# Kernel optimization log

Measured on AMD Instinct MI355X. Metric: run time of the kernel, lower is better.

The kernel has to match this reference:

```python
import jax, jax.numpy as jnp
import numpy as np

# Dimensions pinned by the module: RelPosEmb1DAISummer(tokens=50, dim_head=124)
H = 8          # num_heads
D = 31         # channels // num_heads
T = 4          # time axis of the (p, t) spatial grid; D*T == 124 == dim_head
P = 50         # tokens
C = H * D      # 248 channels
SCALE = D ** -0.5  # note: module scales by d**-0.5 (=31), not (d*t)**-0.5 -- faithful


def rel_to_abs(x):
    """AI-Summer 1D relative->absolute reindexing. x: [b, h, l, 2l-1] -> [b, h, l, l]."""
    b, h, l, _ = x.shape
    x = jnp.pad(x, ((0, 0), (0, 0), (0, 0), (0, 1)))          # [b,h,l,2l]
    x = x.reshape(b, h, l * 2 * l)
    x = jnp.pad(x, ((0, 0), (0, 0), (0, l - 1)))
    x = x.reshape(b, h, l + 1, 2 * l - 1)
    return x[:, :, :l, l - 1:]


def setup_inputs() -> dict:
    key = jax.random.key(0)
    k1, k2, k3, k4 = jax.random.split(key, 4)
    B = 512
    x = jax.random.normal(k1, (B, C, P, T), jnp.float32)
    # 1x1 conv == per-position linear over channels: weight [3C, C], bias [3C]
    w_qkv = jax.random.normal(k2, (3 * C, C), jnp.float32) * (C ** -0.5)
    b_qkv = jax.random.normal(k3, (3 * C,), jnp.float32) * 0.01
    # shared-heads relative position embedding: [2*tokens-1, dim_head]
    rel_emb = jax.random.normal(k4, (2 * P - 1, D * T), jnp.float32) * ((D * T) ** -0.5)
    return {"x": x, "w_qkv": w_qkv, "b_qkv": b_qkv, "rel_emb": rel_emb}


def reference(x, w_qkv, b_qkv, rel_emb):
    B = x.shape[0]
    # 1x1 Conv2d: [B, C, P, T] -> [B, 3C, P, T]
    qkv = jnp.einsum('bcpt,oc->bopt', x, w_qkv) + b_qkv[None, :, None, None]
    # 'b (qkv h d) p t -> qkv b h d p t'
    qkv = qkv.reshape(B, 3, H, D, P, T)
    q, k, v = qkv[:, 0], qkv[:, 1], qkv[:, 2]                 # each [B,H,D,P,T]
    q = q.transpose(0, 1, 3, 2, 4).reshape(B, H, P, D * T)    # 'b h d p t -> b h p (d t)'
    k = k.transpose(0, 1, 2, 4, 3).reshape(B, H, D * T, P)    # 'b h d p t -> b h (d t) p'
    v = v.transpose(0, 1, 3, 2, 4).reshape(B, H, P, D * T)
    dots = jnp.einsum('bhpi,bhiq->bhpq', q, k)                # [B,H,P,P]
    bias = rel_to_abs(jnp.einsum('bhpd,rd->bhpr', q, rel_emb))
    attn = jax.nn.softmax((dots + bias) * SCALE, axis=-1)     # dropout = identity (eval)
    out = jnp.einsum('bhpq,bhqi->bhpi', attn, v)              # [B,H,P,D*T]
    # 'b h p (d t) -> b (h d) p t'
    out = out.reshape(B, H, P, D, T).transpose(0, 1, 3, 2, 4).reshape(B, H * D, P, T)
    return out
```

## Files before the change

### kernel.cpp

```cpp
#include <hip/hip_runtime.h>
#include <hip/hip_bf16.h>

typedef __bf16 bf16_t;
typedef bf16_t bf16x8 __attribute__((ext_vector_type(8)));
typedef bf16_t bf16x4 __attribute__((ext_vector_type(4)));
typedef float f32x4 __attribute__((ext_vector_type(4)));

constexpr float SCALE = 0.17960530202677491f;

#define XT_OFF   0
#define QH_OFF   102400
#define KH_OFF   115200
#define AS_OFF   115200
#define VT_OFF   128000
#define LS_OFF   144384
#define SMEM_BYTES 157984

__device__ __forceinline__ f32x4 mfma16(bf16x8 a, bf16x8 b, f32x4 c) {
    return __builtin_amdgcn_mfma_f32_16x16x32_bf16(a, b, c, 0, 0, 0);
}

__global__ void prep_kernel(const float* __restrict__ w, const float* __restrict__ b_qkv,
                            const float* __restrict__ rel,
                            bf16_t* __restrict__ Wf, bf16_t* __restrict__ relf,
                            float* __restrict__ bp)
{
    int i = blockIdx.x * 256 + threadIdx.x;
    if (i < 196608) {
        int e = i & 7, lane = (i >> 3) & 63;
        int f = i >> 9;
        int ks = f & 7, g = f >> 3;
        int h = g / 6, m = g - h * 6;
        int r15 = lane & 15, g4 = lane >> 4;
        int s = m >> 1, d = ((m & 1) << 4) + r15;
        int c = ks * 32 + g4 * 8 + e;
        float v = 0.f;
        if (d < 31 && c < 248) v = w[(long)(s * 248 + h * 31 + d) * 248 + c];
        Wf[i] = (bf16_t)v;
        return;
    }
    i -= 196608;
    if (i < 14336) {
        int e = i & 7, lane = (i >> 3) & 63;
        int f = i >> 9;
        int ks = f & 3, rt = f >> 2;
        int r = rt * 16 + (lane & 15);
        int dt = ks * 32 + (lane >> 4) * 8 + e;
        float v = 0.f;
        if (r < 99 && dt < 124) v = rel[r * 124 + dt];
        relf[i] = (bf16_t)v;
        return;
    }
    i -= 14336;
    if (i < 768) {
        int h = i / 96, row = i - h * 96;
        int s = row >> 5, d = row & 31;
        bp[i] = (d < 31) ? b_qkv[s * 248 + h * 31 + d] : 0.f;
    }
}

__global__ __launch_bounds__(512, 2)
void fused_kernel(const float* __restrict__ x, const bf16_t* __restrict__ Wf,
                  const bf16_t* __restrict__ relf, const float* __restrict__ bp,
                  float* __restrict__ out)
{
    extern __shared__ char smem[];
    const int b    = blockIdx.x;
    const int tid  = threadIdx.x;
    const int lane = tid & 63;
    const int w    = tid >> 6;
    const int r15  = lane & 15, g4 = lane >> 4;

    {
        *(f32x4*)(smem + VT_OFF + tid * 32)      = f32x4{0.f, 0.f, 0.f, 0.f};
        *(f32x4*)(smem + VT_OFF + tid * 32 + 16) = f32x4{0.f, 0.f, 0.f, 0.f};
        if (tid < 100) {
            int p = tid >> 1;
            int base = (tid & 1) ? KH_OFF : QH_OFF;
            int chunk = 15 ^ (p & 7);
            *(long*)(smem + base + p * 256 + chunk * 16 + 8) = 0L;
        }
        if (tid < 200) {
            int chunk = 31 ^ ((tid >> 2) & 7);
            *(f32x4*)(smem + XT_OFF + tid * 512 + chunk * 16) = f32x4{0.f, 0.f, 0.f, 0.f};
        }
        const float* xb = x + (long)b * 49600;
        const int q = lane;
#pragma unroll 2
        for (int r = 0; r < 31; ++r) {
            int c = w * 31 + r;
            if (q < 50) {
                float4 v = *(const float4*)(xb + c * 200 + q * 4);
                int base = XT_OFF + (4 * q) * 512 + (((c >> 3) ^ (q & 7)) << 4) + (c & 7) * 2;
                *(bf16_t*)(smem + base)        = (bf16_t)v.x;
                *(bf16_t*)(smem + base + 512)  = (bf16_t)v.y;
                *(bf16_t*)(smem + base + 1024) = (bf16_t)v.z;
                *(bf16_t*)(smem + base + 1536) = (bf16_t)v.w;
            }
        }
    }
    __syncthreads();

    const int mu = w >> 2;
    const int nu = w & 3;
    bf16x8 Areg[4][8];
#pragma unroll
    for (int ui = 0; ui < 4; ++ui) {
        int n = (nu * 4 + ui) * 16 + r15;
        int hash = (n >> 2) & 7;
#pragma unroll
        for (int ks = 0; ks < 8; ++ks)
            Areg[ui][ks] = *(const bf16x8*)(smem + XT_OFF + n * 512 + ((((ks << 2) | g4) ^ hash) << 4));
    }
    __syncthreads();

    const int ptile = w >> 1, chalf = w & 1;

    for (int h = 0; h < 8; ++h) {
#pragma unroll
        for (int m3 = 0; m3 < 3; ++m3) {
            int m = mu * 3 + m3;
            int s = m >> 1;
            int d = ((m & 1) << 4) + r15;
            float bias = bp[h * 96 + m * 16 + r15];
            f32x4 acc[4];
#pragma unroll
            for (int ui = 0; ui < 4; ++ui) acc[ui] = f32x4{0.f, 0.f, 0.f, 0.f};
            const bf16_t* wfrag = Wf + ((long)((h * 6 + m) * 8) << 9) + lane * 8;
#pragma unroll
            for (int ks = 0; ks < 8; ++ks) {
                bf16x8 Bf = *(const bf16x8*)(wfrag + (ks << 9));
#pragma unroll
                for (int ui = 0; ui < 4; ++ui)
                    acc[ui] = mfma16(Areg[ui][ks], Bf, acc[ui]);
            }
            if (d < 31) {
#pragma unroll
                for (int ui = 0; ui < 4; ++ui) {
                    int p = (nu * 4 + ui) * 4 + g4;
                    if (p >= 50) continue;
                    float a0 = acc[ui][0] + bias, a1 = acc[ui][1] + bias;
                    float a2 = acc[ui][2] + bias, a3 = acc[ui][3] + bias;
                    if (s < 2) {
                        bf16x4 pk = {(bf16_t)a0, (bf16_t)a1, (bf16_t)a2, (bf16_t)a3};
                        int base = (s == 0) ? QH_OFF : KH_OFF;
                        int chunk = (d >> 1) ^ (p & 7);
                        *(bf16x4*)(smem + base + p * 256 + chunk * 16 + ((d & 1) << 3)) = pk;
                    } else {
                        int chunk = ((p >> 3) ^ (d & 7)) << 4;
                        int vbase = VT_OFF + (d * 4) * 128 + chunk + (p & 7) * 2;
                        *(bf16_t*)(smem + vbase)       = (bf16_t)a0;
                        *(bf16_t*)(smem + vbase + 128) = (bf16_t)a1;
                        *(bf16_t*)(smem + vbase + 256) = (bf16_t)a2;
                        *(bf16_t*)(smem + vbase + 384) = (bf16_t)a3;
                    }
                }
            }
        }
        __syncthreads();

        bf16x8 Afr[4];
        {
            int p = ptile * 16 + r15;
            int hp = p & 7;
#pragma unroll
            for (int ks = 0; ks < 4; ++ks)
                Afr[ks] = *(const bf16x8*)(smem + QH_OFF + p * 256 + ((((ks << 2) | g4) ^ hp) << 4));
        }
        f32x4 sacc[6];
#pragma unroll
        for (int i = 0; i < 6; ++i) sacc[i] = f32x4{0.f, 0.f, 0.f, 0.f};
        const int nct = chalf ? 5 : 6;
        const int ct0 = chalf ? 6 : 0;
        for (int i = 0; i < nct; ++i) {
            int ct = ct0 + i;
            if (ct < 4) {
                int c = ct * 16 + r15;
                int hc = c & 7;
#pragma unroll
                for (int ks = 0; ks < 4; ++ks) {
                    bf16x8 Bf = *(const bf16x8*)(smem + KH_OFF + c * 256 + ((((ks << 2) | g4) ^ hc) << 4));
                    sacc[i] = mfma16(Afr[ks], Bf, sacc[i]);
                }
            } else {
                const bf16_t* rf = relf + (((ct - 4) * 4) << 9) + lane * 8;
#pragma unroll
                for (int ks = 0; ks < 4; ++ks) {
                    bf16x8 Bf = *(const bf16x8*)(rf + (ks << 9));
                    sacc[i] = mfma16(Afr[ks], Bf, sacc[i]);
                }
            }
        }
        if (chalf == 0) {
#pragma unroll
            for (int i = 0; i < 4; ++i) {
                int c = i * 16 + r15;
                if (c < 50) {
#pragma unroll
                    for (int j = 0; j < 4; ++j) {
                        int qrow = ptile * 16 + g4 * 4 + j;
                        if (qrow < 50)
                            *(float*)(smem + LS_OFF + (qrow * 68 + c) * 4) = sacc[i][j];
                    }
                }
            }
        }
        __syncthreads();
        for (int i = 0; i < nct; ++i) {
            int ct = ct0 + i;
            if (ct < 4) continue;
            int r = ct * 16 + r15 - 64;
#pragma unroll
            for (int j = 0; j < 4; ++j) {
                int qrow = ptile * 16 + g4 * 4 + j;
                int jj = r + qrow - 49;
                if (qrow < 50 && jj >= 0 && jj < 50) {
                    float* pL = (float*)(smem + LS_OFF + (qrow * 68 + jj) * 4);
                    *pL += sacc[i][j];
                }
            }
        }
        __syncthreads();
        {
            int row = tid >> 3, sub = tid & 7;
            if (row < 50) {
                float mx = -1e30f;
                for (int jj = sub; jj < 50; jj += 8)
                    mx = fmaxf(mx, *(const float*)(smem + LS_OFF + (row * 68 + jj) * 4));
                mx = fmaxf(mx, __shfl_xor(mx, 1));
                mx = fmaxf(mx, __shfl_xor(mx, 2));
                mx = fmaxf(mx, __shfl_xor(mx, 4));
                float sum = 0.f;
                for (int jj = sub; jj < 50; jj += 8) {
                    float* pL = (float*)(smem + LS_OFF + (row * 68 + jj) * 4);
                    float e = __expf((*pL - mx) * SCALE);
                    *pL = e;
                    sum += e;
                }
                sum += __shfl_xor(sum, 1);
                sum += __shfl_xor(sum, 2);
                sum += __shfl_xor(sum, 4);
                float rs = 1.f / sum;
                int hrow = row & 7;
                for (int jj = sub; jj < 64; jj += 8) {
                    float v = 0.f;
                    if (jj < 50)
                        v = *(const float*)(smem + LS_OFF + (row * 68 + jj) * 4) * rs;
                    *(bf16_t*)(smem + AS_OFF + row * 128 + (((jj >> 3) ^ hrow) << 4) + (jj & 7) * 2) = (bf16_t)v;
                }
            }
        }
        __syncthreads();
        {
            bf16x8 Av[2];
            int irow = w * 16 + r15;
            int hv = (irow >> 2) & 7;
#pragma unroll
            for (int ks = 0; ks < 2; ++ks)
                Av[ks] = *(const bf16x8*)(smem + VT_OFF + irow * 128 + ((((ks << 2) | g4) ^ hv) << 4));
            int dd = w * 4 + g4;
#pragma unroll
            for (int pt = 0; pt < 4; ++pt) {
                f32x4 po = f32x4{0.f, 0.f, 0.f, 0.f};
                int prow = pt * 16 + r15;
                int hp = prow & 7;
#pragma unroll
                for (int ks = 0; ks < 2; ++ks) {
                    bf16x8 Bs = *(const bf16x8*)(smem + AS_OFF + prow * 128 + ((((ks << 2) | g4) ^ hp) << 4));
                    po = mfma16(Av[ks], Bs, po);
                }
                if (dd < 31 && prow < 50) {
                    *(f32x4*)(out + ((long)b * 248 + h * 31 + dd) * 200 + prow * 4) = po;
                }
            }
        }
        __syncthreads();
    }
}

extern "C" void kernel_launch(void* const* d_in, const int* in_sizes, int n_in,
                              void* d_out, int out_size, void* d_ws, size_t ws_size,
                              hipStream_t stream)
{
    const float* x   = (const float*)d_in[0];
    const float* wq  = (const float*)d_in[1];
    const float* bq  = (const float*)d_in[2];
    const float* rel = (const float*)d_in[3];
    float* out = (float*)d_out;

    char* ws = (char*)d_ws;
    bf16_t* Wf   = (bf16_t*)ws;
    bf16_t* relf = (bf16_t*)(ws + 393216);
    float*  bp   = (float*)(ws + 421888);

    const int B = in_sizes[0] / 49600;

    static int smem_set = -1;
    (void)smem_set;
    hipFuncSetAttribute((const void*)fused_kernel,
                        hipFuncAttributeMaxDynamicSharedMemorySize, SMEM_BYTES);

    prep_kernel<<<dim3(828), dim3(256), 0, stream>>>(wq, bq, rel, Wf, relf, bp);
    fused_kernel<<<dim3(B), dim3(512), SMEM_BYTES, stream>>>(x, Wf, relf, bp, out);
}
```

Before: 231.0 us.

## Double block to 1024 threads and repartition per-head work across 16 waves

Launches the fused attention kernel with 1024 threads (16 waves) per batch item instead of 512 and splits every per-head stage more finely: each wave now computes 2 instead of 4 QKV row tiles, one score column tile plus up to two relative-position tiles, and half as many output tiles. The x staging is rewritten so each thread gathers 8 channels for one (p,t) position and writes a packed bf16x8 to LDS with a new swizzle, and the extra barrier after loading A fragments is removed. The intent is to cut per-wave serial MFMA and softmax work and raise latency hiding. In exchange, register budget per thread is tighter and more waves contend at each barrier; with about 154 KB of LDS per block, occupancy is still one block per CU.

```diff
diff --git a/kernel.cpp b/kernel.cpp
--- a/kernel.cpp
+++ b/kernel.cpp
@@ -59,7 +59,7 @@
     }
 }
 
-__global__ __launch_bounds__(512, 2)
+__global__ __launch_bounds__(1024, 4)
 void fused_kernel(const float* __restrict__ x, const bf16_t* __restrict__ Wf,
                   const bf16_t* __restrict__ relf, const float* __restrict__ bp,
                   float* __restrict__ out)
@@ -71,50 +71,52 @@
     const int w    = tid >> 6;
     const int r15  = lane & 15, g4 = lane >> 4;
 
+    *(f32x4*)(smem + VT_OFF + tid * 16) = f32x4{0.f, 0.f, 0.f, 0.f};
+    if (tid < 100) {
+        int p = tid >> 1;
+        int base = (tid & 1) ? KH_OFF : QH_OFF;
+        int chunk = 15 ^ (p & 7);
+        *(long*)(smem + base + p * 256 + chunk * 16 + 8) = 0L;
+    }
     {
-        *(f32x4*)(smem + VT_OFF + tid * 32)      = f32x4{0.f, 0.f, 0.f, 0.f};
-        *(f32x4*)(smem + VT_OFF + tid * 32 + 16) = f32x4{0.f, 0.f, 0.f, 0.f};
-        if (tid < 100) {
-            int p = tid >> 1;
-            int base = (tid & 1) ? KH_OFF : QH_OFF;
-            int chunk = 15 ^ (p & 7);
-            *(long*)(smem + base + p * 256 + chunk * 16 + 8) = 0L;
-        }
-        if (tid < 200) {
-            int chunk = 31 ^ ((tid >> 2) & 7);
-            *(f32x4*)(smem + XT_OFF + tid * 512 + chunk * 16) = f32x4{0.f, 0.f, 0.f, 0.f};
-        }
-        const float* xb = x + (long)b * 49600;
-        const int q = lane;
-#pragma unroll 2
-        for (int r = 0; r < 31; ++r) {
-            int c = w * 31 + r;
-            if (q < 50) {
-                float4 v = *(const float4*)(xb + c * 200 + q * 4);
-                int base = XT_OFF + (4 * q) * 512 + (((c >> 3) ^ (q & 7)) << 4) + (c & 7) * 2;
-                *(bf16_t*)(smem + base)        = (bf16_t)v.x;
-                *(bf16_t*)(smem + base + 512)  = (bf16_t)v.y;
-                *(bf16_t*)(smem + base + 1024) = (bf16_t)v.z;
-                *(bf16_t*)(smem + base + 1536) = (bf16_t)v.w;
+        const int n  = tid & 255;
+        const int cg = tid >> 8;
+        if (n < 200) {
+            const float* xb = x + (long)b * 49600 + n;
+            const int hash = (n >> 1) & 7;
+#pragma unroll
+            for (int cb = 0; cb < 8; ++cb) {
+                bf16x8 pk;
+#pragma unroll
+                for (int e = 0; e < 8; ++e) {
+                    int c = cg * 64 + cb * 8 + e;
+                    float v = (c < 248) ? xb[(long)c * 200] : 0.f;
+                    pk[e] = (bf16_t)v;
+                }
+                *(bf16x8*)(smem + XT_OFF + n * 512 + (((cg * 8 + cb) ^ hash) << 4)) = pk;
             }
         }
     }
     __syncthreads();
 
-    const int mu = w >> 2;
-    const int nu = w & 3;
-    bf16x8 Areg[4][8];
-#pragma unroll
-    for (int ui = 0; ui < 4; ++ui) {
-        int n = (nu * 4 + ui) * 16 + r15;
-        int hash = (n >> 2) & 7;
-#pragma unroll
-        for (int ks = 0; ks < 8; ++ks)
-            Areg[ui][ks] = *(const bf16x8*)(smem + XT_OFF + n * 512 + ((((ks << 2) | g4) ^ hash) << 4));
-    }
-    __syncthreads();
-
-    const int ptile = w >> 1, chalf = w & 1;
+    const int mu = w >> 3;
+    const int nu = w & 7;
+    bf16x8 Areg[2][8];
+#pragma unroll
+    for (int ui = 0; ui < 2; ++ui) {
+        int n = (nu * 2 + ui) * 16 + r15;
+        int hash = (n >> 1) & 7;
+#pragma unroll
+        for (int ks = 0; ks < 8; ++ks) {
+            bf16x8 v = {};
+            if (n < 200)
+                v = *(const bf16x8*)(smem + XT_OFF + n * 512 + ((((ks << 2) | g4) ^ hash) << 4));
+            Areg[ui][ks] = v;
+        }
+    }
+
+    const int ptile = w >> 2, cq = w & 3;
+    const int it = w >> 1, psel = w & 1;
 
     for (int h = 0; h < 8; ++h) {
 #pragma unroll
@@ -123,24 +125,23 @@
             int s = m >> 1;
             int d = ((m & 1) << 4) + r15;
             float bias = bp[h * 96 + m * 16 + r15];
-            f32x4 acc[4];
-#pragma unroll
-            for (int ui = 0; ui < 4; ++ui) acc[ui] = f32x4{0.f, 0.f, 0.f, 0.f};
+            f32x4 acc0 = f32x4{0.f, 0.f, 0.f, 0.f};
+            f32x4 acc1 = f32x4{0.f, 0.f, 0.f, 0.f};
             const bf16_t* wfrag = Wf + ((long)((h * 6 + m) * 8) << 9) + lane * 8;
 #pragma unroll
             for (int ks = 0; ks < 8; ++ks) {
                 bf16x8 Bf = *(const bf16x8*)(wfrag + (ks << 9));
-#pragma unroll
-                for (int ui = 0; ui < 4; ++ui)
-                    acc[ui] = mfma16(Areg[ui][ks], Bf, acc[ui]);
+                acc0 = mfma16(Areg[0][ks], Bf, acc0);
+                acc1 = mfma16(Areg[1][ks], Bf, acc1);
             }
             if (d < 31) {
 #pragma unroll
-                for (int ui = 0; ui < 4; ++ui) {
-                    int p = (nu * 4 + ui) * 4 + g4;
+                for (int ui = 0; ui < 2; ++ui) {
+                    f32x4 a = ui ? acc1 : acc0;
+                    int p = (nu * 2 + ui) * 4 + g4;
                     if (p >= 50) continue;
-                    float a0 = acc[ui][0] + bias, a1 = acc[ui][1] + bias;
-                    float a2 = acc[ui][2] + bias, a3 = acc[ui][3] + bias;
+                    float a0 = a[0] + bias, a1 = a[1] + bias;
+                    float a2 = a[2] + bias, a3 = a[3] + bias;
                     if (s < 2) {
                         bf16x4 pk = {(bf16_t)a0, (bf16_t)a1, (bf16_t)a2, (bf16_t)a3};
                         int base = (s == 0) ? QH_OFF : KH_OFF;
@@ -167,71 +168,79 @@
             for (int ks = 0; ks < 4; ++ks)
                 Afr[ks] = *(const bf16x8*)(smem + QH_OFF + p * 256 + ((((ks << 2) | g4) ^ hp) << 4));
         }
-        f32x4 sacc[6];
-#pragma unroll
-        for (int i = 0; i < 6; ++i) sacc[i] = f32x4{0.f, 0.f, 0.f, 0.f};
-        const int nct = chalf ? 5 : 6;
-        const int ct0 = chalf ? 6 : 0;
-        for (int i = 0; i < nct; ++i) {
-            int ct = ct0 + i;
-            if (ct < 4) {
-                int c = ct * 16 + r15;
-                int hc = c & 7;
-#pragma unroll
-                for (int ks = 0; ks < 4; ++ks) {
-                    bf16x8 Bf = *(const bf16x8*)(smem + KH_OFF + c * 256 + ((((ks << 2) | g4) ^ hc) << 4));
-                    sacc[i] = mfma16(Afr[ks], Bf, sacc[i]);
-                }
-            } else {
-                const bf16_t* rf = relf + (((ct - 4) * 4) << 9) + lane * 8;
-#pragma unroll
-                for (int ks = 0; ks < 4; ++ks) {
-                    bf16x8 Bf = *(const bf16x8*)(rf + (ks << 9));
-                    sacc[i] = mfma16(Afr[ks], Bf, sacc[i]);
-                }
-            }
-        }
-        if (chalf == 0) {
-#pragma unroll
-            for (int i = 0; i < 4; ++i) {
-                int c = i * 16 + r15;
-                if (c < 50) {
-#pragma unroll
-                    for (int j = 0; j < 4; ++j) {
-                        int qrow = ptile * 16 + g4 * 4 + j;
-                        if (qrow < 50)
-                            *(float*)(smem + LS_OFF + (qrow * 68 + c) * 4) = sacc[i][j];
-                    }
-                }
-            }
-        }
-        __syncthreads();
-        for (int i = 0; i < nct; ++i) {
-            int ct = ct0 + i;
-            if (ct < 4) continue;
-            int r = ct * 16 + r15 - 64;
+        f32x4 s0 = f32x4{0.f, 0.f, 0.f, 0.f};
+        f32x4 s1 = f32x4{0.f, 0.f, 0.f, 0.f};
+        f32x4 s2 = f32x4{0.f, 0.f, 0.f, 0.f};
+        {
+            int c = cq * 16 + r15;
+            int hc = c & 7;
+#pragma unroll
+            for (int ks = 0; ks < 4; ++ks) {
+                bf16x8 Bf = *(const bf16x8*)(smem + KH_OFF + c * 256 + ((((ks << 2) | g4) ^ hc) << 4));
+                s0 = mfma16(Afr[ks], Bf, s0);
+            }
+        }
+        {
+            const bf16_t* rf = relf + ((long)(cq * 4) << 9) + lane * 8;
+#pragma unroll
+            for (int ks = 0; ks < 4; ++ks) {
+                bf16x8 Bf = *(const bf16x8*)(rf + (ks << 9));
+                s1 = mfma16(Afr[ks], Bf, s1);
+            }
+        }
+        if (cq < 3) {
+            const bf16_t* rf = relf + ((long)((cq + 4) * 4) << 9) + lane * 8;
+#pragma unroll
+            for (int ks = 0; ks < 4; ++ks) {
+                bf16x8 Bf = *(const bf16x8*)(rf + (ks << 9));
+                s2 = mfma16(Afr[ks], Bf, s2);
+            }
+        }
+        {
+            int c = cq * 16 + r15;
+            if (c < 50) {
+#pragma unroll
+                for (int j = 0; j < 4; ++j) {
+                    int qrow = ptile * 16 + g4 * 4 + j;
+                    if (qrow < 50)
+                        *(float*)(smem + LS_OFF + (qrow * 68 + c) * 4) = s0[j];
+                }
+            }
+        }
+        __syncthreads();
+        {
+            int r = cq * 16 + r15;
 #pragma unroll
             for (int j = 0; j < 4; ++j) {
                 int qrow = ptile * 16 + g4 * 4 + j;
                 int jj = r + qrow - 49;
-                if (qrow < 50 && jj >= 0 && jj < 50) {
-                    float* pL = (float*)(smem + LS_OFF + (qrow * 68 + jj) * 4);
-                    *pL += sacc[i][j];
-                }
-            }
-        }
-        __syncthreads();
-        {
-            int row = tid >> 3, sub = tid & 7;
+                if (qrow < 50 && jj >= 0 && jj < 50)
+                    *(float*)(smem + LS_OFF + (qrow * 68 + jj) * 4) += s1[j];
+            }
+        }
+        if (cq < 3) {
+            int r = (cq + 4) * 16 + r15;
+#pragma unroll
+            for (int j = 0; j < 4; ++j) {
+                int qrow = ptile * 16 + g4 * 4 + j;
+                int jj = r + qrow - 49;
+                if (qrow < 50 && jj >= 0 && jj < 50)
+                    *(float*)(smem + LS_OFF + (qrow * 68 + jj) * 4) += s2[j];
+            }
+        }
+        __syncthreads();
+        {
+            int row = tid >> 4, sub = tid & 15;
             if (row < 50) {
                 float mx = -1e30f;
-                for (int jj = sub; jj < 50; jj += 8)
+                for (int jj = sub; jj < 50; jj += 16)
                     mx = fmaxf(mx, *(const float*)(smem + LS_OFF + (row * 68 + jj) * 4));
                 mx = fmaxf(mx, __shfl_xor(mx, 1));
                 mx = fmaxf(mx, __shfl_xor(mx, 2));
                 mx = fmaxf(mx, __shfl_xor(mx, 4));
+                mx = fmaxf(mx, __shfl_xor(mx, 8));
                 float sum = 0.f;
-                for (int jj = sub; jj < 50; jj += 8) {
+                for (int jj = sub; jj < 50; jj += 16) {
                     float* pL = (float*)(smem + LS_OFF + (row * 68 + jj) * 4);
                     float e = __expf((*pL - mx) * SCALE);
                     *pL = e;
@@ -240,9 +249,10 @@
                 sum += __shfl_xor(sum, 1);
                 sum += __shfl_xor(sum, 2);
                 sum += __shfl_xor(sum, 4);
+                sum += __shfl_xor(sum, 8);
                 float rs = 1.f / sum;
                 int hrow = row & 7;
-                for (int jj = sub; jj < 64; jj += 8) {
+                for (int jj = sub; jj < 64; jj += 16) {
                     float v = 0.f;
                     if (jj < 50)
                         v = *(const float*)(smem + LS_OFF + (row * 68 + jj) * 4) * rs;
@@ -253,25 +263,25 @@
         __syncthreads();
         {
             bf16x8 Av[2];
-            int irow = w * 16 + r15;
+            int irow = it * 16 + r15;
             int hv = (irow >> 2) & 7;
 #pragma unroll
             for (int ks = 0; ks < 2; ++ks)
                 Av[ks] = *(const bf16x8*)(smem + VT_OFF + irow * 128 + ((((ks << 2) | g4) ^ hv) << 4));
-            int dd = w * 4 + g4;
-#pragma unroll
-            for (int pt = 0; pt < 4; ++pt) {
+            int dd = it * 4 + g4;
+#pragma unroll
+            for (int pi = 0; pi < 2; ++pi) {
+                int pt = psel * 2 + pi;
+                int prow = pt * 16 + r15;
+                int hp2 = prow & 7;
                 f32x4 po = f32x4{0.f, 0.f, 0.f, 0.f};
-                int prow = pt * 16 + r15;
-                int hp = prow & 7;
 #pragma unroll
                 for (int ks = 0; ks < 2; ++ks) {
-                    bf16x8 Bs = *(const bf16x8*)(smem + AS_OFF + prow * 128 + ((((ks << 2) | g4) ^ hp) << 4));
+                    bf16x8 Bs = *(const bf16x8*)(smem + AS_OFF + prow * 128 + ((((ks << 2) | g4) ^ hp2) << 4));
                     po = mfma16(Av[ks], Bs, po);
                 }
-                if (dd < 31 && prow < 50) {
+                if (dd < 31 && prow < 50)
                     *(f32x4*)(out + ((long)b * 248 + h * 31 + dd) * 200 + prow * 4) = po;
-                }
             }
         }
         __syncthreads();
@@ -295,11 +305,9 @@
 
     const int B = in_sizes[0] / 49600;
 
-    static int smem_set = -1;
-    (void)smem_set;
     hipFuncSetAttribute((const void*)fused_kernel,
                         hipFuncAttributeMaxDynamicSharedMemorySize, SMEM_BYTES);
 
     prep_kernel<<<dim3(828), dim3(256), 0, stream>>>(wq, bq, rel, Wf, relf, bp);
-    fused_kernel<<<dim3(B), dim3(512), SMEM_BYTES, stream>>>(x, Wf, relf, bp, out);
+    fused_kernel<<<dim3(B), dim3(1024), SMEM_BYTES, stream>>>(x, Wf, relf, bp, out);
 }
```

New measurement: 306.4 us. +32.7%, slower.

## Shrink block to four waves, load x directly into registers, drop X staging

Applied to the files above, without the earlier changes.

Block size drops from 512 to 256 threads, with each wave owning a 16-row query tile end to end. The x tile now goes straight from global memory into MFMA A-fragments (strided scalar loads) instead of being staged in LDS. This removes the large XT buffer, cutting LDS from about 158KB to static arrays of about 70KB so more blocks can be resident. Wave-local lgkmcnt fences replace two block barriers in the score/bias/softmax phase, and W and rel fragments are software double-buffered. The risks are uncoalesced strided global loads for x, higher register pressure from the prefetch buffers, and half as many waves per block to hide latency.

```diff
diff --git a/kernel.cpp b/kernel.cpp
--- a/kernel.cpp
+++ b/kernel.cpp
@@ -8,16 +8,12 @@
 
 constexpr float SCALE = 0.17960530202677491f;
 
-#define XT_OFF   0
-#define QH_OFF   102400
-#define KH_OFF   115200
-#define AS_OFF   115200
-#define VT_OFF   128000
-#define LS_OFF   144384
-#define SMEM_BYTES 157984
-
 __device__ __forceinline__ f32x4 mfma16(bf16x8 a, bf16x8 b, f32x4 c) {
     return __builtin_amdgcn_mfma_f32_16x16x32_bf16(a, b, c, 0, 0, 0);
+}
+
+__device__ __forceinline__ void wave_lds_fence() {
+    asm volatile("s_waitcnt lgkmcnt(0)" ::: "memory");
 }
 
 __global__ void prep_kernel(const float* __restrict__ w, const float* __restrict__ b_qkv,
@@ -59,12 +55,17 @@
     }
 }
 
-__global__ __launch_bounds__(512, 2)
+__global__ __launch_bounds__(256, 2)
 void fused_kernel(const float* __restrict__ x, const bf16_t* __restrict__ Wf,
                   const bf16_t* __restrict__ relf, const float* __restrict__ bp,
                   float* __restrict__ out)
 {
-    extern __shared__ char smem[];
+    __shared__ __align__(16) bf16_t QH[64][128];
+    __shared__ __align__(16) bf16_t KH[64][128];
+    __shared__ __align__(16) bf16_t AS[64][64];
+    __shared__ __align__(16) bf16_t VT[128][64];
+    __shared__ float LS[50][68];
+
     const int b    = blockIdx.x;
     const int tid  = threadIdx.x;
     const int lane = tid & 63;
@@ -72,206 +73,191 @@
     const int r15  = lane & 15, g4 = lane >> 4;
 
     {
-        *(f32x4*)(smem + VT_OFF + tid * 32)      = f32x4{0.f, 0.f, 0.f, 0.f};
-        *(f32x4*)(smem + VT_OFF + tid * 32 + 16) = f32x4{0.f, 0.f, 0.f, 0.f};
-        if (tid < 100) {
-            int p = tid >> 1;
-            int base = (tid & 1) ? KH_OFF : QH_OFF;
-            int chunk = 15 ^ (p & 7);
-            *(long*)(smem + base + p * 256 + chunk * 16 + 8) = 0L;
-        }
-        if (tid < 200) {
-            int chunk = 31 ^ ((tid >> 2) & 7);
-            *(f32x4*)(smem + XT_OFF + tid * 512 + chunk * 16) = f32x4{0.f, 0.f, 0.f, 0.f};
-        }
-        const float* xb = x + (long)b * 49600;
-        const int q = lane;
-#pragma unroll 2
-        for (int r = 0; r < 31; ++r) {
-            int c = w * 31 + r;
-            if (q < 50) {
-                float4 v = *(const float4*)(xb + c * 200 + q * 4);
-                int base = XT_OFF + (4 * q) * 512 + (((c >> 3) ^ (q & 7)) << 4) + (c & 7) * 2;
-                *(bf16_t*)(smem + base)        = (bf16_t)v.x;
-                *(bf16_t*)(smem + base + 512)  = (bf16_t)v.y;
-                *(bf16_t*)(smem + base + 1024) = (bf16_t)v.z;
-                *(bf16_t*)(smem + base + 1536) = (bf16_t)v.w;
-            }
-        }
-    }
-    __syncthreads();
-
-    const int mu = w >> 2;
-    const int nu = w & 3;
+        *(f32x4*)((char*)&VT[0][0] + tid * 64)      = f32x4{0.f, 0.f, 0.f, 0.f};
+        *(f32x4*)((char*)&VT[0][0] + tid * 64 + 16) = f32x4{0.f, 0.f, 0.f, 0.f};
+        *(f32x4*)((char*)&VT[0][0] + tid * 64 + 32) = f32x4{0.f, 0.f, 0.f, 0.f};
+        *(f32x4*)((char*)&VT[0][0] + tid * 64 + 48) = f32x4{0.f, 0.f, 0.f, 0.f};
+        if (tid < 128) {
+            int row = tid & 63;
+            char* base = (tid < 64) ? (char*)&QH[0][0] : (char*)&KH[0][0];
+            int chunk = 15 ^ (row & 7);
+            *(long*)(base + row * 256 + chunk * 16 + 8) = 0L;
+        }
+    }
+
+    const float* xb = x + (long)b * 49600;
     bf16x8 Areg[4][8];
 #pragma unroll
     for (int ui = 0; ui < 4; ++ui) {
-        int n = (nu * 4 + ui) * 16 + r15;
-        int hash = (n >> 2) & 7;
+        int n = w * 64 + ui * 16 + r15;
+        const float* xn = xb + n;
+        bool nok = (n < 200);
+#pragma unroll
+        for (int ks = 0; ks < 8; ++ks) {
+            bf16x8 fr;
+#pragma unroll
+            for (int e = 0; e < 8; ++e) {
+                int c = ks * 32 + g4 * 8 + e;
+                float v = (nok && c < 248) ? xn[(long)c * 200] : 0.f;
+                fr[e] = (bf16_t)v;
+            }
+            Areg[ui][ks] = fr;
+        }
+    }
+
+    for (int h = 0; h < 8; ++h) {
+        const bf16_t* wf = Wf + ((long)(h * 48) << 9) + lane * 8;
+        bf16x8 Bc[8], Bn[8];
 #pragma unroll
         for (int ks = 0; ks < 8; ++ks)
-            Areg[ui][ks] = *(const bf16x8*)(smem + XT_OFF + n * 512 + ((((ks << 2) | g4) ^ hash) << 4));
-    }
-    __syncthreads();
-
-    const int ptile = w >> 1, chalf = w & 1;
-
-    for (int h = 0; h < 8; ++h) {
-#pragma unroll
-        for (int m3 = 0; m3 < 3; ++m3) {
-            int m = mu * 3 + m3;
+            Bc[ks] = *(const bf16x8*)(wf + (ks << 9));
+#pragma unroll
+        for (int m = 0; m < 6; ++m) {
+            if (m < 5) {
+#pragma unroll
+                for (int ks = 0; ks < 8; ++ks)
+                    Bn[ks] = *(const bf16x8*)(wf + (((m + 1) * 8 + ks) << 9));
+            }
+            f32x4 acc[4];
+#pragma unroll
+            for (int ui = 0; ui < 4; ++ui) acc[ui] = f32x4{0.f, 0.f, 0.f, 0.f};
+#pragma unroll
+            for (int ks = 0; ks < 8; ++ks)
+#pragma unroll
+                for (int ui = 0; ui < 4; ++ui)
+                    acc[ui] = mfma16(Areg[ui][ks], Bc[ks], acc[ui]);
+
             int s = m >> 1;
             int d = ((m & 1) << 4) + r15;
             float bias = bp[h * 96 + m * 16 + r15];
-            f32x4 acc[4];
-#pragma unroll
-            for (int ui = 0; ui < 4; ++ui) acc[ui] = f32x4{0.f, 0.f, 0.f, 0.f};
-            const bf16_t* wfrag = Wf + ((long)((h * 6 + m) * 8) << 9) + lane * 8;
-#pragma unroll
-            for (int ks = 0; ks < 8; ++ks) {
-                bf16x8 Bf = *(const bf16x8*)(wfrag + (ks << 9));
-#pragma unroll
-                for (int ui = 0; ui < 4; ++ui)
-                    acc[ui] = mfma16(Areg[ui][ks], Bf, acc[ui]);
-            }
             if (d < 31) {
 #pragma unroll
                 for (int ui = 0; ui < 4; ++ui) {
-                    int p = (nu * 4 + ui) * 4 + g4;
+                    int p = (w * 4 + ui) * 4 + g4;
                     if (p >= 50) continue;
                     float a0 = acc[ui][0] + bias, a1 = acc[ui][1] + bias;
                     float a2 = acc[ui][2] + bias, a3 = acc[ui][3] + bias;
                     if (s < 2) {
                         bf16x4 pk = {(bf16_t)a0, (bf16_t)a1, (bf16_t)a2, (bf16_t)a3};
-                        int base = (s == 0) ? QH_OFF : KH_OFF;
+                        char* base = (s == 0) ? (char*)&QH[0][0] : (char*)&KH[0][0];
                         int chunk = (d >> 1) ^ (p & 7);
-                        *(bf16x4*)(smem + base + p * 256 + chunk * 16 + ((d & 1) << 3)) = pk;
+                        *(bf16x4*)(base + p * 256 + chunk * 16 + ((d & 1) << 3)) = pk;
                     } else {
                         int chunk = ((p >> 3) ^ (d & 7)) << 4;
-                        int vbase = VT_OFF + (d * 4) * 128 + chunk + (p & 7) * 2;
-                        *(bf16_t*)(smem + vbase)       = (bf16_t)a0;
-                        *(bf16_t*)(smem + vbase + 128) = (bf16_t)a1;
-                        *(bf16_t*)(smem + vbase + 256) = (bf16_t)a2;
-                        *(bf16_t*)(smem + vbase + 384) = (bf16_t)a3;
+                        char* vbase = (char*)&VT[0][0] + (d * 4) * 128 + chunk + (p & 7) * 2;
+                        *(bf16_t*)(vbase)       = (bf16_t)a0;
+                        *(bf16_t*)(vbase + 128) = (bf16_t)a1;
+                        *(bf16_t*)(vbase + 256) = (bf16_t)a2;
+                        *(bf16_t*)(vbase + 384) = (bf16_t)a3;
                     }
                 }
             }
+#pragma unroll
+            for (int ks = 0; ks < 8; ++ks) Bc[ks] = Bn[ks];
         }
         __syncthreads();
 
         bf16x8 Afr[4];
         {
-            int p = ptile * 16 + r15;
+            int p = w * 16 + r15;
             int hp = p & 7;
 #pragma unroll
             for (int ks = 0; ks < 4; ++ks)
-                Afr[ks] = *(const bf16x8*)(smem + QH_OFF + p * 256 + ((((ks << 2) | g4) ^ hp) << 4));
-        }
-        f32x4 sacc[6];
-#pragma unroll
-        for (int i = 0; i < 6; ++i) sacc[i] = f32x4{0.f, 0.f, 0.f, 0.f};
-        const int nct = chalf ? 5 : 6;
-        const int ct0 = chalf ? 6 : 0;
-        for (int i = 0; i < nct; ++i) {
-            int ct = ct0 + i;
-            if (ct < 4) {
-                int c = ct * 16 + r15;
-                int hc = c & 7;
-#pragma unroll
-                for (int ks = 0; ks < 4; ++ks) {
-                    bf16x8 Bf = *(const bf16x8*)(smem + KH_OFF + c * 256 + ((((ks << 2) | g4) ^ hc) << 4));
-                    sacc[i] = mfma16(Afr[ks], Bf, sacc[i]);
-                }
-            } else {
-                const bf16_t* rf = relf + (((ct - 4) * 4) << 9) + lane * 8;
-#pragma unroll
-                for (int ks = 0; ks < 4; ++ks) {
-                    bf16x8 Bf = *(const bf16x8*)(rf + (ks << 9));
-                    sacc[i] = mfma16(Afr[ks], Bf, sacc[i]);
-                }
-            }
-        }
-        if (chalf == 0) {
-#pragma unroll
-            for (int i = 0; i < 4; ++i) {
-                int c = i * 16 + r15;
-                if (c < 50) {
-#pragma unroll
-                    for (int j = 0; j < 4; ++j) {
-                        int qrow = ptile * 16 + g4 * 4 + j;
-                        if (qrow < 50)
-                            *(float*)(smem + LS_OFF + (qrow * 68 + c) * 4) = sacc[i][j];
-                    }
-                }
-            }
-        }
-        __syncthreads();
-        for (int i = 0; i < nct; ++i) {
-            int ct = ct0 + i;
-            if (ct < 4) continue;
-            int r = ct * 16 + r15 - 64;
-#pragma unroll
-            for (int j = 0; j < 4; ++j) {
-                int qrow = ptile * 16 + g4 * 4 + j;
-                int jj = r + qrow - 49;
-                if (qrow < 50 && jj >= 0 && jj < 50) {
-                    float* pL = (float*)(smem + LS_OFF + (qrow * 68 + jj) * 4);
-                    *pL += sacc[i][j];
-                }
-            }
-        }
-        __syncthreads();
+                Afr[ks] = *(const bf16x8*)((char*)&QH[0][0] + p * 256 + ((((ks << 2) | g4) ^ hp) << 4));
+        }
+#pragma unroll
+        for (int ct = 0; ct < 4; ++ct) {
+            int c = ct * 16 + r15;
+            int hc = c & 7;
+            f32x4 s = f32x4{0.f, 0.f, 0.f, 0.f};
+#pragma unroll
+            for (int ks = 0; ks < 4; ++ks) {
+                bf16x8 Bf = *(const bf16x8*)((char*)&KH[0][0] + c * 256 + ((((ks << 2) | g4) ^ hc) << 4));
+                s = mfma16(Afr[ks], Bf, s);
+            }
+            if (c < 50) {
+#pragma unroll
+                for (int j = 0; j < 4; ++j) {
+                    int qrow = w * 16 + g4 * 4 + j;
+                    if (qrow < 50) LS[qrow][c] = s[j];
+                }
+            }
+        }
+        wave_lds_fence();
         {
-            int row = tid >> 3, sub = tid & 7;
+            const bf16_t* rf = relf + lane * 8;
+            bf16x8 R0[4], R1[4];
+#pragma unroll
+            for (int ks = 0; ks < 4; ++ks) R0[ks] = *(const bf16x8*)(rf + (ks << 9));
+            for (int rt = 0; rt < 7; ++rt) {
+                if (rt < 6) {
+#pragma unroll
+                    for (int ks = 0; ks < 4; ++ks)
+                        R1[ks] = *(const bf16x8*)(rf + (((rt + 1) * 4 + ks) << 9));
+                }
+                f32x4 s = f32x4{0.f, 0.f, 0.f, 0.f};
+#pragma unroll
+                for (int ks = 0; ks < 4; ++ks) s = mfma16(Afr[ks], R0[ks], s);
+                int r = rt * 16 + r15;
+#pragma unroll
+                for (int j = 0; j < 4; ++j) {
+                    int qrow = w * 16 + g4 * 4 + j;
+                    int jj = r + qrow - 49;
+                    if (qrow < 50 && jj >= 0 && jj < 50) LS[qrow][jj] += s[j];
+                }
+#pragma unroll
+                for (int ks = 0; ks < 4; ++ks) R0[ks] = R1[ks];
+            }
+        }
+        wave_lds_fence();
+        {
+            int row = w * 16 + (lane >> 2);
+            int quad = lane & 3;
             if (row < 50) {
                 float mx = -1e30f;
-                for (int jj = sub; jj < 50; jj += 8)
-                    mx = fmaxf(mx, *(const float*)(smem + LS_OFF + (row * 68 + jj) * 4));
+                for (int jj = quad; jj < 50; jj += 4) mx = fmaxf(mx, LS[row][jj]);
                 mx = fmaxf(mx, __shfl_xor(mx, 1));
                 mx = fmaxf(mx, __shfl_xor(mx, 2));
-                mx = fmaxf(mx, __shfl_xor(mx, 4));
                 float sum = 0.f;
-                for (int jj = sub; jj < 50; jj += 8) {
-                    float* pL = (float*)(smem + LS_OFF + (row * 68 + jj) * 4);
-                    float e = __expf((*pL - mx) * SCALE);
-                    *pL = e;
+                for (int jj = quad; jj < 50; jj += 4) {
+                    float e = __expf((LS[row][jj] - mx) * SCALE);
+                    LS[row][jj] = e;
                     sum += e;
                 }
                 sum += __shfl_xor(sum, 1);
                 sum += __shfl_xor(sum, 2);
-                sum += __shfl_xor(sum, 4);
                 float rs = 1.f / sum;
                 int hrow = row & 7;
-                for (int jj = sub; jj < 64; jj += 8) {
-                    float v = 0.f;
-                    if (jj < 50)
-                        v = *(const float*)(smem + LS_OFF + (row * 68 + jj) * 4) * rs;
-                    *(bf16_t*)(smem + AS_OFF + row * 128 + (((jj >> 3) ^ hrow) << 4) + (jj & 7) * 2) = (bf16_t)v;
+                for (int jj = quad; jj < 64; jj += 4) {
+                    float v = (jj < 50) ? LS[row][jj] * rs : 0.f;
+                    *(bf16_t*)((char*)&AS[0][0] + row * 128 + (((jj >> 3) ^ hrow) << 4) + (jj & 7) * 2) = (bf16_t)v;
                 }
             }
         }
         __syncthreads();
-        {
+
+#pragma unroll
+        for (int ii = 0; ii < 2; ++ii) {
+            int it = w * 2 + ii;
+            int irow = it * 16 + r15;
+            int hv = (irow >> 2) & 7;
             bf16x8 Av[2];
-            int irow = w * 16 + r15;
-            int hv = (irow >> 2) & 7;
 #pragma unroll
             for (int ks = 0; ks < 2; ++ks)
-                Av[ks] = *(const bf16x8*)(smem + VT_OFF + irow * 128 + ((((ks << 2) | g4) ^ hv) << 4));
-            int dd = w * 4 + g4;
+                Av[ks] = *(const bf16x8*)((char*)&VT[0][0] + irow * 128 + ((((ks << 2) | g4) ^ hv) << 4));
+            int dd = it * 4 + g4;
 #pragma unroll
             for (int pt = 0; pt < 4; ++pt) {
+                int prow = pt * 16 + r15;
+                int hp2 = prow & 7;
                 f32x4 po = f32x4{0.f, 0.f, 0.f, 0.f};
-                int prow = pt * 16 + r15;
-                int hp = prow & 7;
 #pragma unroll
                 for (int ks = 0; ks < 2; ++ks) {
-                    bf16x8 Bs = *(const bf16x8*)(smem + AS_OFF + prow * 128 + ((((ks << 2) | g4) ^ hp) << 4));
+                    bf16x8 Bs = *(const bf16x8*)((char*)&AS[0][0] + prow * 128 + ((((ks << 2) | g4) ^ hp2) << 4));
                     po = mfma16(Av[ks], Bs, po);
                 }
-                if (dd < 31 && prow < 50) {
+                if (dd < 31 && prow < 50)
                     *(f32x4*)(out + ((long)b * 248 + h * 31 + dd) * 200 + prow * 4) = po;
-                }
             }
         }
         __syncthreads();
@@ -295,11 +281,6 @@
 
     const int B = in_sizes[0] / 49600;
 
-    static int smem_set = -1;
-    (void)smem_set;
-    hipFuncSetAttribute((const void*)fused_kernel,
-                        hipFuncAttributeMaxDynamicSharedMemorySize, SMEM_BYTES);
-
     prep_kernel<<<dim3(828), dim3(256), 0, stream>>>(wq, bq, rel, Wf, relf, bp);
-    fused_kernel<<<dim3(B), dim3(512), SMEM_BYTES, stream>>>(x, Wf, relf, bp, out);
-}
+    fused_kernel<<<dim3(B), dim3(256), 0, stream>>>(x, Wf, relf, bp, out);
+}
```

Measured after the change: 254.0 us. 10.0% more time.
